# Kernel tuning notes

Hardware: AMD Instinct MI355X
Metric: run time of the kernel (lower is better)

## Reference

```python
import jax, jax.numpy as jnp
import numpy as np

BN_EPS = 1e-5


def spmm(rows, cols, vals, x):
    # Sparse [V,V] @ x for x: [B, V, F]. COO (rows, cols, vals) with E nnz.
    B, V, F = x.shape
    xt = jnp.transpose(x, (1, 0, 2)).reshape(V, B * F)      # [V, B*F]
    msg = xt[cols] * vals[:, None]                           # [E, B*F]
    y = jax.ops.segment_sum(msg, rows, num_segments=V)       # [V, B*F]
    return jnp.transpose(y.reshape(V, B, F), (1, 0, 2))      # [B, V, F]


def cheb_conv(rows, cols, vals, x, W, b):
    # Chebyshev graph conv: out = sum_k T_k(L) x @ W[k] + b ; W: [K, Fin, Fout]
    K = W.shape[0]
    x0 = x
    out = jnp.einsum('bvi,io->bvo', x0, W[0])
    if K > 1:
        x1 = spmm(rows, cols, vals, x0)
        out = out + jnp.einsum('bvi,io->bvo', x1, W[1])
        for k in range(2, K):
            x2 = 2.0 * spmm(rows, cols, vals, x1) - x0
            out = out + jnp.einsum('bvi,io->bvo', x2, W[k])
            x0, x1 = x1, x2
    return out + b


def bn_relu(x, gamma, beta):
    # BatchNorm1d (training stats) over (batch, nodes) per channel, then ReLU.
    m = jnp.mean(x, axis=(0, 1))
    v = jnp.var(x, axis=(0, 1))
    y = (x - m) * jax.lax.rsqrt(v + BN_EPS) * gamma + beta
    return jax.nn.relu(y)


def setup_inputs() -> dict:
    key = jax.random.key(0)
    ks = jax.random.split(key, 8)
    V, DEG, B, CIN, COUT = 49152, 20, 2, 128, 64
    x = jax.random.normal(ks[0], (B, V, CIN), dtype=jnp.float32)
    # HEALPix-like sparse Laplacian: diagonal + 20 random neighbors per node
    self_idx = jnp.arange(V, dtype=jnp.int32)
    nbr = jax.random.randint(ks[1], (V * DEG,), 0, V, dtype=jnp.int32)
    rows = jnp.concatenate([self_idx, jnp.repeat(self_idx, DEG)])
    cols = jnp.concatenate([self_idx, nbr])
    vals = jax.random.normal(ks[2], (V * (DEG + 1),), dtype=jnp.float32) * 0.1
    def w(k, shape):
        fan_in = shape[0] * shape[1]
        return jax.random.normal(k, shape, dtype=jnp.float32) * np.float32(np.sqrt(2.0 / fan_in))
    return {
        'x': x, 'rows': rows, 'cols': cols, 'vals': vals,
        'W1': w(ks[3], (1, CIN, COUT)), 'b1': jnp.zeros((COUT,), jnp.float32),
        'g1': jnp.ones((COUT,), jnp.float32), 'be1': jnp.zeros((COUT,), jnp.float32),
        'W2': w(ks[4], (3, COUT, COUT)), 'b2': jnp.zeros((COUT,), jnp.float32),
        'g2': jnp.ones((COUT,), jnp.float32), 'be2': jnp.zeros((COUT,), jnp.float32),
        'W3': w(ks[5], (1, COUT, CIN)), 'b3': jnp.zeros((CIN,), jnp.float32),
        'g3': jnp.ones((CIN,), jnp.float32), 'be3': jnp.zeros((CIN,), jnp.float32),
    }


def reference(x, rows, cols, vals, W1, b1, g1, be1, W2, b2, g2, be2, W3, b3, g3, be3):
    h = bn_relu(cheb_conv(rows, cols, vals, x, W1, b1), g1, be1)   # [B,V,64]
    h = bn_relu(cheb_conv(rows, cols, vals, h, W2, b2), g2, be2)   # [B,V,64]
    h = bn_relu(cheb_conv(rows, cols, vals, h, W3, b3), g3, be3)   # [B,V,128]
    return h
```

## Files before the change

### kernel.cpp

```cpp
#include <hip/hip_runtime.h>

#define VN 49152
#define DEG 20
#define NB 2
#define MROWS (NB * VN)

static constexpr float BN_EPS = 1e-5f;

typedef short bf16x8 __attribute__((ext_vector_type(8)));
typedef float floatx4 __attribute__((ext_vector_type(4)));

__device__ __forceinline__ unsigned short f2bf(float f) {
  unsigned int u = __builtin_bit_cast(unsigned int, f);
  u += 0x7FFFu + ((u >> 16) & 1u);
  return (unsigned short)(u >> 16);
}
__device__ __forceinline__ float bf2f(unsigned short h) {
  unsigned int u = ((unsigned int)h) << 16;
  return __builtin_bit_cast(float, u);
}
__device__ __forceinline__ float bflo(unsigned int u) {
  return __builtin_bit_cast(float, u << 16);
}
__device__ __forceinline__ float bfhi(unsigned int u) {
  return __builtin_bit_cast(float, u & 0xFFFF0000u);
}
__device__ __forceinline__ unsigned int packbf(float a, float b) {
  return (unsigned int)f2bf(a) | ((unsigned int)f2bf(b) << 16);
}


#define LDA1 136
__global__ __launch_bounds__(256) void gemm1(const float* __restrict__ X,
    const float* __restrict__ W, const float* __restrict__ bias,
    unsigned short* __restrict__ Y, float* __restrict__ part) {
  __shared__ unsigned short As[128 * LDA1];
  __shared__ unsigned short Bs[64 * LDA1];
  __shared__ float sred[128];
  int t = threadIdx.x;
  int row0 = blockIdx.x * 128;
  if (t < 128) sred[t] = 0.f;
  const float* Xt = X + (size_t)row0 * 128;
  #pragma unroll
  for (int c = 0; c < 16; ++c) {
    int f4i = c * 256 + t;
    int row = f4i >> 5, k = (f4i & 31) * 4;
    float4 v = *(const float4*)(Xt + row * 128 + k);
    unsigned int p0 = packbf(v.x, v.y);
    unsigned int p1 = packbf(v.z, v.w);
    *(uint2*)(&As[row * LDA1 + k]) = make_uint2(p0, p1);
  }
  #pragma unroll
  for (int c = 0; c < 32; ++c) {
    int f = c * 256 + t;
    int k = f >> 6, n = f & 63;
    Bs[n * LDA1 + k] = f2bf(W[f]);
  }
  __syncthreads();
  int l = t & 63, wv = t >> 6;
  int lr = l & 15, q = l >> 4;
  int m0 = wv * 32;
  floatx4 acc[2][4];
  #pragma unroll
  for (int mi = 0; mi < 2; ++mi)
    #pragma unroll
    for (int ni = 0; ni < 4; ++ni) acc[mi][ni] = (floatx4)(0.f);
  #pragma unroll
  for (int ks = 0; ks < 128; ks += 32) {
    bf16x8 af[2], bfr[4];
    #pragma unroll
    for (int mi = 0; mi < 2; ++mi)
      af[mi] = *(const bf16x8*)(&As[(m0 + mi * 16 + lr) * LDA1 + ks + q * 8]);
    #pragma unroll
    for (int ni = 0; ni < 4; ++ni)
      bfr[ni] = *(const bf16x8*)(&Bs[(ni * 16 + lr) * LDA1 + ks + q * 8]);
    #pragma unroll
    for (int mi = 0; mi < 2; ++mi)
      #pragma unroll
      for (int ni = 0; ni < 4; ++ni)
        acc[mi][ni] = __builtin_amdgcn_mfma_f32_16x16x32_bf16(af[mi], bfr[ni], acc[mi][ni], 0, 0, 0);
  }
  int b = (row0 >= VN) ? 1 : 0;
  int vbase = row0 - b * VN + m0;
  #pragma unroll
  for (int ni = 0; ni < 4; ++ni) {
    int col = ni * 16 + lr;
    float bv = bias[col];
    size_t sub = (size_t)(b * 2 + (col >> 5)) * VN;
    float s = 0.f, s2 = 0.f;
    #pragma unroll
    for (int mi = 0; mi < 2; ++mi)
      #pragma unroll
      for (int r = 0; r < 4; ++r) {
        float y = acc[mi][ni][r] + bv;
        s += y; s2 += y * y;
        int v = vbase + mi * 16 + q * 4 + r;
        Y[(sub + v) * 32 + (col & 31)] = f2bf(y);
      }
    atomicAdd(&sred[col], s);
    atomicAdd(&sred[64 + col], s2);
  }
  __syncthreads();
  if (t < 128) part[(size_t)blockIdx.x * 128 + t] = sred[t];
}

#define LDA2 72
__global__ __launch_bounds__(256) void gemm2(const unsigned short* __restrict__ X0,
    const unsigned short* __restrict__ X1, const unsigned short* __restrict__ X2,
    const float* __restrict__ W, const float* __restrict__ bias,
    unsigned short* __restrict__ Y, float* __restrict__ part) {
  __shared__ unsigned short As[128 * LDA2];
  __shared__ unsigned short Bs[64 * LDA2];
  __shared__ float sred[128];
  int t = threadIdx.x;
  int row0 = blockIdx.x * 128;
  int b = (row0 >= VN) ? 1 : 0;
  int b2 = b * 2;
  int vb0 = row0 - b * VN;
  if (t < 128) sred[t] = 0.f;
  int l = t & 63, wv = t >> 6;
  int lr = l & 15, q = l >> 4;
  int m0 = wv * 32;
  floatx4 acc[2][4];
  #pragma unroll
  for (int mi = 0; mi < 2; ++mi)
    #pragma unroll
    for (int ni = 0; ni < 4; ++ni) acc[mi][ni] = (floatx4)(0.f);

  for (int term = 0; term < 3; ++term) {
    const unsigned short* Xp = (term == 0) ? X0 : (term == 1) ? X1 : X2;
    const float* Wt = W + term * 64 * 64;
    #pragma unroll
    for (int c8 = 0; c8 < 8; ++c8) {
      int i = c8 * 256 + t;
      int row = i >> 4, k = (i & 15) * 4;
      const unsigned short* src = Xp + ((size_t)(b2 + (k >> 5)) * VN + vb0 + row) * 32 + (k & 31);
      *(uint2*)(&As[row * LDA2 + k]) = *(const uint2*)src;
    }
    #pragma unroll
    for (int c = 0; c < 16; ++c) {
      int f = c * 256 + t;
      int k = f >> 6, n = f & 63;
      Bs[n * LDA2 + k] = f2bf(Wt[f]);
    }
    __syncthreads();
    #pragma unroll
    for (int ks = 0; ks < 64; ks += 32) {
      bf16x8 af[2], bfr[4];
      #pragma unroll
      for (int mi = 0; mi < 2; ++mi)
        af[mi] = *(const bf16x8*)(&As[(m0 + mi * 16 + lr) * LDA2 + ks + q * 8]);
      #pragma unroll
      for (int ni = 0; ni < 4; ++ni)
        bfr[ni] = *(const bf16x8*)(&Bs[(ni * 16 + lr) * LDA2 + ks + q * 8]);
      #pragma unroll
      for (int mi = 0; mi < 2; ++mi)
        #pragma unroll
        for (int ni = 0; ni < 4; ++ni)
          acc[mi][ni] = __builtin_amdgcn_mfma_f32_16x16x32_bf16(af[mi], bfr[ni], acc[mi][ni], 0, 0, 0);
    }
    __syncthreads();
  }
  int vbase = vb0 + m0;
  #pragma unroll
  for (int ni = 0; ni < 4; ++ni) {
    int col = ni * 16 + lr;
    float bv = bias[col];
    size_t sub = (size_t)(b2 + (col >> 5)) * VN;
    float s = 0.f, s2 = 0.f;
    #pragma unroll
    for (int mi = 0; mi < 2; ++mi)
      #pragma unroll
      for (int r = 0; r < 4; ++r) {
        float y = acc[mi][ni][r] + bv;
        s += y; s2 += y * y;
        int v = vbase + mi * 16 + q * 4 + r;
        Y[(sub + v) * 32 + (col & 31)] = f2bf(y);
      }
    atomicAdd(&sred[col], s);
    atomicAdd(&sred[64 + col], s2);
  }
  __syncthreads();
  if (t < 128) part[(size_t)blockIdx.x * 128 + t] = sred[t];
}

__global__ __launch_bounds__(256) void gemm3(const unsigned short* __restrict__ X,
    const float* __restrict__ W, const float* __restrict__ bias,
    const float* __restrict__ scsh, unsigned short* __restrict__ Y,
    float* __restrict__ part) {
  __shared__ unsigned short As[128 * LDA2];
  __shared__ unsigned short Bs[64 * LDA2];
  __shared__ float sred[128];
  int t = threadIdx.x;
  int row0 = blockIdx.x * 128;
  int n0 = blockIdx.y * 64;
  int b = (row0 >= VN) ? 1 : 0;
  int b2 = b * 2;
  int vb0 = row0 - b * VN;
  if (t < 128) sred[t] = 0.f;
  #pragma unroll
  for (int c8 = 0; c8 < 8; ++c8) {
    int i = c8 * 256 + t;
    int row = i >> 4, k = (i & 15) * 4;
    const unsigned short* src = X + ((size_t)(b2 + (k >> 5)) * VN + vb0 + row) * 32 + (k & 31);
    uint2 rawv = *(const uint2*)src;
    float y0 = fmaf(bflo(rawv.x), scsh[k + 0], scsh[64 + k + 0]);
    float y1 = fmaf(bfhi(rawv.x), scsh[k + 1], scsh[64 + k + 1]);
    float y2 = fmaf(bflo(rawv.y), scsh[k + 2], scsh[64 + k + 2]);
    float y3 = fmaf(bfhi(rawv.y), scsh[k + 3], scsh[64 + k + 3]);
    y0 = y0 > 0.f ? y0 : 0.f; y1 = y1 > 0.f ? y1 : 0.f;
    y2 = y2 > 0.f ? y2 : 0.f; y3 = y3 > 0.f ? y3 : 0.f;
    *(uint2*)(&As[row * LDA2 + k]) = make_uint2(packbf(y0, y1), packbf(y2, y3));
  }
  #pragma unroll
  for (int c = 0; c < 16; ++c) {
    int f = c * 256 + t;
    int k = f >> 6, n = f & 63;
    Bs[n * LDA2 + k] = f2bf(W[k * 128 + n0 + n]);
  }
  __syncthreads();
  int l = t & 63, wv = t >> 6;
  int lr = l & 15, q = l >> 4;
  int m0 = wv * 32;
  floatx4 acc[2][4];
  #pragma unroll
  for (int mi = 0; mi < 2; ++mi)
    #pragma unroll
    for (int ni = 0; ni < 4; ++ni) acc[mi][ni] = (floatx4)(0.f);
  #pragma unroll
  for (int ks = 0; ks < 64; ks += 32) {
    bf16x8 af[2], bfr[4];
    #pragma unroll
    for (int mi = 0; mi < 2; ++mi)
      af[mi] = *(const bf16x8*)(&As[(m0 + mi * 16 + lr) * LDA2 + ks + q * 8]);
    #pragma unroll
    for (int ni = 0; ni < 4; ++ni)
      bfr[ni] = *(const bf16x8*)(&Bs[(ni * 16 + lr) * LDA2 + ks + q * 8]);
    #pragma unroll
    for (int mi = 0; mi < 2; ++mi)
      #pragma unroll
      for (int ni = 0; ni < 4; ++ni)
        acc[mi][ni] = __builtin_amdgcn_mfma_f32_16x16x32_bf16(af[mi], bfr[ni], acc[mi][ni], 0, 0, 0);
  }
  #pragma unroll
  for (int ni = 0; ni < 4; ++ni) {
    int lc = ni * 16 + lr;
    int col = n0 + lc;
    float bv = bias[col];
    float s = 0.f, s2 = 0.f;
    #pragma unroll
    for (int mi = 0; mi < 2; ++mi)
      #pragma unroll
      for (int r = 0; r < 4; ++r) {
        float y = acc[mi][ni][r] + bv;
        s += y; s2 += y * y;
        int row = row0 + m0 + mi * 16 + q * 4 + r;
        Y[(size_t)row * 128 + col] = f2bf(y);
      }
    atomicAdd(&sred[lc], s);
    atomicAdd(&sred[64 + lc], s2);
  }
  __syncthreads();
  if (t < 128)
    part[((size_t)blockIdx.y * 768 + blockIdx.x) * 128 + t] = sred[t];
}

__global__ __launch_bounds__(128) void reduce_scsh64(const float* __restrict__ part,
    const float* __restrict__ gamma, const float* __restrict__ beta,
    float* __restrict__ scsh) {
  int t = threadIdx.x;
  const float* p = part + t;
  float a0 = 0.f, a1 = 0.f, a2 = 0.f, a3 = 0.f;
  for (int b = 0; b < 768; b += 4) {
    a0 += p[(size_t)(b + 0) * 128]; a1 += p[(size_t)(b + 1) * 128];
    a2 += p[(size_t)(b + 2) * 128]; a3 += p[(size_t)(b + 3) * 128];
  }
  __shared__ float sm[128];
  sm[t] = (a0 + a1) + (a2 + a3);
  __syncthreads();
  if (t < 64) {
    float mean = sm[t] * (1.f / MROWS);
    float var = sm[64 + t] * (1.f / MROWS) - mean * mean;
    float sc = gamma[t] * rsqrtf(var + BN_EPS);
    scsh[t] = sc;
    scsh[64 + t] = beta[t] - mean * sc;
  }
}

__global__ __launch_bounds__(256) void reduce_scsh128(const float* __restrict__ part,
    const float* __restrict__ gamma, const float* __restrict__ beta,
    float* __restrict__ scsh) {
  int t = threadIdx.x;
  int col = t & 127, s = t >> 7;
  int gy = col >> 6, lc = col & 63;
  const float* p = part + (size_t)gy * 768 * 128 + s * 64 + lc;
  float a0 = 0.f, a1 = 0.f, a2 = 0.f, a3 = 0.f;
  for (int gx = 0; gx < 768; gx += 4) {
    a0 += p[(size_t)(gx + 0) * 128]; a1 += p[(size_t)(gx + 1) * 128];
    a2 += p[(size_t)(gx + 2) * 128]; a3 += p[(size_t)(gx + 3) * 128];
  }
  __shared__ float sm[256];
  sm[s * 128 + col] = (a0 + a1) + (a2 + a3);
  __syncthreads();
  if (t < 128) {
    float mean = sm[t] * (1.f / MROWS);
    float var = sm[128 + t] * (1.f / MROWS) - mean * mean;
    float sc = gamma[t] * rsqrtf(var + BN_EPS);
    scsh[t] = sc;
    scsh[128 + t] = beta[t] - mean * sc;
  }
}

__global__ __launch_bounds__(256) void bn_h1(const unsigned short* __restrict__ T1,
    const float* __restrict__ scsh, unsigned short* __restrict__ H1) {
  int g = blockIdx.x;
  int combo = (g & 7) >> 1;
  int rg = ((g >> 3) << 1) | (g & 1);
  int t = threadIdx.x;
  int wv = t >> 6, lane = t & 63;
  int v = rg * 64 + wv * 16 + (lane >> 2);
  int ch0 = (lane & 3) * 8;
  int cb = (combo & 1) * 32 + ch0;
  size_t off = (size_t)combo * VN * 32 + (size_t)v * 32 + ch0;
  uint4 d = *(const uint4*)(T1 + off);
  float y[8];
  y[0] = fmaf(bflo(d.x), scsh[cb + 0], scsh[64 + cb + 0]);
  y[1] = fmaf(bfhi(d.x), scsh[cb + 1], scsh[64 + cb + 1]);
  y[2] = fmaf(bflo(d.y), scsh[cb + 2], scsh[64 + cb + 2]);
  y[3] = fmaf(bfhi(d.y), scsh[cb + 3], scsh[64 + cb + 3]);
  y[4] = fmaf(bflo(d.z), scsh[cb + 4], scsh[64 + cb + 4]);
  y[5] = fmaf(bfhi(d.z), scsh[cb + 5], scsh[64 + cb + 5]);
  y[6] = fmaf(bflo(d.w), scsh[cb + 6], scsh[64 + cb + 6]);
  y[7] = fmaf(bfhi(d.w), scsh[cb + 7], scsh[64 + cb + 7]);
  #pragma unroll
  for (int j = 0; j < 8; ++j) y[j] = y[j] > 0.f ? y[j] : 0.f;
  uint4 o;
  o.x = packbf(y[0], y[1]); o.y = packbf(y[2], y[3]);
  o.z = packbf(y[4], y[5]); o.w = packbf(y[6], y[7]);
  *(uint4*)(H1 + off) = o;
}

__global__ __launch_bounds__(256) void spmm1(const unsigned short* __restrict__ H1,
    const int* __restrict__ cols, const float* __restrict__ vals,
    unsigned short* __restrict__ X1out) {
  int g = blockIdx.x;
  int combo = (g & 7) >> 1;
  int rg = ((g >> 3) << 1) | (g & 1);
  int t = threadIdx.x;
  int wv = t >> 6, lane = t & 63;
  int v = rg * 64 + wv * 16 + (lane >> 2);
  int ch0 = (lane & 3) * 8;
  const unsigned short* __restrict__ plane = H1 + (size_t)combo * VN * 32;
  float a[8];
  {
    float w0 = vals[v];
    uint4 d = *(const uint4*)(plane + (size_t)v * 32 + ch0);
    a[0] = w0 * bflo(d.x); a[1] = w0 * bfhi(d.x);
    a[2] = w0 * bflo(d.y); a[3] = w0 * bfhi(d.y);
    a[4] = w0 * bflo(d.z); a[5] = w0 * bfhi(d.z);
    a[6] = w0 * bflo(d.w); a[7] = w0 * bfhi(d.w);
  }
  const int*   __restrict__ cp = cols + VN + v * DEG;
  const float* __restrict__ vp = vals + VN + v * DEG;
  #pragma unroll
  for (int j = 0; j < DEG; ++j) {
    int cj = cp[j];
    float wj = vp[j];
    uint4 d = *(const uint4*)(plane + (size_t)cj * 32 + ch0);
    a[0] = fmaf(bflo(d.x), wj, a[0]); a[1] = fmaf(bfhi(d.x), wj, a[1]);
    a[2] = fmaf(bflo(d.y), wj, a[2]); a[3] = fmaf(bfhi(d.y), wj, a[3]);
    a[4] = fmaf(bflo(d.z), wj, a[4]); a[5] = fmaf(bfhi(d.z), wj, a[5]);
    a[6] = fmaf(bflo(d.w), wj, a[6]); a[7] = fmaf(bfhi(d.w), wj, a[7]);
  }
  uint4 o;
  o.x = packbf(a[0], a[1]); o.y = packbf(a[2], a[3]);
  o.z = packbf(a[4], a[5]); o.w = packbf(a[6], a[7]);
  *(uint4*)(X1out + (size_t)combo * VN * 32 + (size_t)v * 32 + ch0) = o;
}

__global__ __launch_bounds__(256) void spmm2(const unsigned short* __restrict__ X1,
    const unsigned short* __restrict__ H1, const int* __restrict__ cols,
    const float* __restrict__ vals, unsigned short* __restrict__ X2out) {
  int g = blockIdx.x;
  int combo = (g & 7) >> 1;
  int rg = ((g >> 3) << 1) | (g & 1);
  int t = threadIdx.x;
  int wv = t >> 6, lane = t & 63;
  int v = rg * 64 + wv * 16 + (lane >> 2);
  int ch0 = (lane & 3) * 8;
  const size_t pbase = (size_t)combo * VN * 32;
  const size_t myoff = pbase + (size_t)v * 32 + ch0;
  const unsigned short* __restrict__ plane = X1 + pbase;
  float a[8];
  {
    float w0 = vals[v];
    uint4 d = *(const uint4*)(X1 + myoff);
    a[0] = w0 * bflo(d.x); a[1] = w0 * bfhi(d.x);
    a[2] = w0 * bflo(d.y); a[3] = w0 * bfhi(d.y);
    a[4] = w0 * bflo(d.z); a[5] = w0 * bfhi(d.z);
    a[6] = w0 * bflo(d.w); a[7] = w0 * bfhi(d.w);
  }
  const int*   __restrict__ cp = cols + VN + v * DEG;
  const float* __restrict__ vp = vals + VN + v * DEG;
  #pragma unroll
  for (int j = 0; j < DEG; ++j) {
    int cj = cp[j];
    float wj = vp[j];
    uint4 d = *(const uint4*)(plane + (size_t)cj * 32 + ch0);
    a[0] = fmaf(bflo(d.x), wj, a[0]); a[1] = fmaf(bfhi(d.x), wj, a[1]);
    a[2] = fmaf(bflo(d.y), wj, a[2]); a[3] = fmaf(bfhi(d.y), wj, a[3]);
    a[4] = fmaf(bflo(d.z), wj, a[4]); a[5] = fmaf(bfhi(d.z), wj, a[5]);
    a[6] = fmaf(bflo(d.w), wj, a[6]); a[7] = fmaf(bfhi(d.w), wj, a[7]);
  }
  uint4 h = *(const uint4*)(H1 + myoff);
  float hh[8] = {bflo(h.x), bfhi(h.x), bflo(h.y), bfhi(h.y),
                 bflo(h.z), bfhi(h.z), bflo(h.w), bfhi(h.w)};
  uint4 o;
  o.x = packbf(2.f * a[0] - hh[0], 2.f * a[1] - hh[1]);
  o.y = packbf(2.f * a[2] - hh[2], 2.f * a[3] - hh[3]);
  o.z = packbf(2.f * a[4] - hh[4], 2.f * a[5] - hh[5]);
  o.w = packbf(2.f * a[6] - hh[6], 2.f * a[7] - hh[7]);
  *(uint4*)(X2out + myoff) = o;
}

__global__ __launch_bounds__(256) void bn_apply_final(const unsigned short* __restrict__ T,
    float* __restrict__ Y, const float* __restrict__ scsh) {
  size_t i4 = ((size_t)blockIdx.x * 256 + threadIdx.x) * 4;
  int c0 = (int)(i4 & 127);
  ushort4 tv = *(const ushort4*)(T + i4);
  unsigned short sv[4] = {tv.x, tv.y, tv.z, tv.w};
  float ov[4];
  #pragma unroll
  for (int j = 0; j < 4; ++j) {
    int c = c0 + j;
    float y = fmaf(bf2f(sv[j]), scsh[c], scsh[128 + c]);
    ov[j] = y > 0.f ? y : 0.f;
  }
  *(float4*)(Y + i4) = make_float4(ov[0], ov[1], ov[2], ov[3]);
}

extern "C" void kernel_launch(void* const* d_in, const int* in_sizes, int n_in,
                              void* d_out, int out_size, void* d_ws, size_t ws_size,
                              hipStream_t stream) {
  const float* x    = (const float*)d_in[0];
  const int*   cols = (const int*)  d_in[2];
  const float* vals = (const float*)d_in[3];
  const float* W1   = (const float*)d_in[4];
  const float* b1   = (const float*)d_in[5];
  const float* g1   = (const float*)d_in[6];
  const float* be1  = (const float*)d_in[7];
  const float* W2   = (const float*)d_in[8];
  const float* b2   = (const float*)d_in[9];
  const float* g2   = (const float*)d_in[10];
  const float* be2  = (const float*)d_in[11];
  const float* W3   = (const float*)d_in[12];
  const float* b3   = (const float*)d_in[13];
  const float* g3   = (const float*)d_in[14];
  const float* be3  = (const float*)d_in[15];
  float* out = (float*)d_out;

  const size_t PL = (size_t)MROWS * 64;
  unsigned short* P0 = (unsigned short*)d_ws;
  unsigned short* PH = P0 + PL;
  unsigned short* P1 = PH + PL;
  unsigned short* P2 = P1 + PL;
  float* part  = (float*)(P2 + 2 * PL);
  float* scsh1 = part + 1536 * 128;
  float* scsh2 = scsh1 + 128;
  float* scsh3 = scsh2 + 128;

  dim3 blk(256);
  int rowb = MROWS / 128;
  int spmm_blocks = 3072;
  int ap128_blocks = (int)(PL * 2 / 4 / 256);

  gemm1<<<rowb, blk, 0, stream>>>(x, W1, b1, P0, part);
  reduce_scsh64<<<1, 128, 0, stream>>>(part, g1, be1, scsh1);
  bn_h1<<<spmm_blocks, blk, 0, stream>>>(P0, scsh1, PH);

  spmm1<<<spmm_blocks, blk, 0, stream>>>(PH, cols, vals, P1);
  spmm2<<<spmm_blocks, blk, 0, stream>>>(P1, PH, cols, vals, P2);
  gemm2<<<rowb, blk, 0, stream>>>(PH, P1, P2, W2, b2, P0, part);
  reduce_scsh64<<<1, 128, 0, stream>>>(part, g2, be2, scsh2);

  dim3 g3grid(rowb, 2);
  gemm3<<<g3grid, blk, 0, stream>>>(P0, W3, b3, scsh2, P2, part);
  reduce_scsh128<<<1, 256, 0, stream>>>(part, g3, be3, scsh3);
  bn_apply_final<<<ap128_blocks, blk, 0, stream>>>(P2, out, scsh3);
}
```

Measured before the change: 285.8 us.

## Fuse BN statistics and BN-ReLU application into the GEMM and SpMM kernels

Each GEMM now reduces its BN statistics with global atomics, and the last block to finish computes scale and shift. This removes the separate reduce kernels and the per-block partials buffer. The standalone bn_h1 pass is dropped: spmm1, spmm2 and gemm2 apply BN+ReLU on the fly to the raw GEMM1 output, so the normalized buffer is never written or read again. gemm3 now computes all 128 output columns per block instead of splitting them over two grid columns, which avoids loading the A tile twice. In exchange, spmm1 redoes the BN+ReLU arithmetic on every gathered neighbor. Float atomics make the summation order nondeterministic, and gemm2 writes its output in place over one of its own inputs.

```diff
diff --git a/kernel.cpp b/kernel.cpp
--- a/kernel.cpp
+++ b/kernel.cpp
@@ -33,10 +33,13 @@
 #define LDA1 136
 __global__ __launch_bounds__(256) void gemm1(const float* __restrict__ X,
     const float* __restrict__ W, const float* __restrict__ bias,
-    unsigned short* __restrict__ Y, float* __restrict__ part) {
+    const float* __restrict__ gamma, const float* __restrict__ beta,
+    unsigned short* __restrict__ Y, float* __restrict__ gsum,
+    int* __restrict__ counter, float* __restrict__ scshOut) {
   __shared__ unsigned short As[128 * LDA1];
   __shared__ unsigned short Bs[64 * LDA1];
   __shared__ float sred[128];
+  __shared__ int amLast;
   int t = threadIdx.x;
   int row0 = blockIdx.x * 128;
   if (t < 128) sred[t] = 0.f;
@@ -101,218 +104,27 @@
     atomicAdd(&sred[64 + col], s2);
   }
   __syncthreads();
-  if (t < 128) part[(size_t)blockIdx.x * 128 + t] = sred[t];
-}
-
-#define LDA2 72
-__global__ __launch_bounds__(256) void gemm2(const unsigned short* __restrict__ X0,
-    const unsigned short* __restrict__ X1, const unsigned short* __restrict__ X2,
-    const float* __restrict__ W, const float* __restrict__ bias,
-    unsigned short* __restrict__ Y, float* __restrict__ part) {
-  __shared__ unsigned short As[128 * LDA2];
-  __shared__ unsigned short Bs[64 * LDA2];
-  __shared__ float sred[128];
-  int t = threadIdx.x;
-  int row0 = blockIdx.x * 128;
-  int b = (row0 >= VN) ? 1 : 0;
-  int b2 = b * 2;
-  int vb0 = row0 - b * VN;
-  if (t < 128) sred[t] = 0.f;
-  int l = t & 63, wv = t >> 6;
-  int lr = l & 15, q = l >> 4;
-  int m0 = wv * 32;
-  floatx4 acc[2][4];
-  #pragma unroll
-  for (int mi = 0; mi < 2; ++mi)
-    #pragma unroll
-    for (int ni = 0; ni < 4; ++ni) acc[mi][ni] = (floatx4)(0.f);
-
-  for (int term = 0; term < 3; ++term) {
-    const unsigned short* Xp = (term == 0) ? X0 : (term == 1) ? X1 : X2;
-    const float* Wt = W + term * 64 * 64;
-    #pragma unroll
-    for (int c8 = 0; c8 < 8; ++c8) {
-      int i = c8 * 256 + t;
-      int row = i >> 4, k = (i & 15) * 4;
-      const unsigned short* src = Xp + ((size_t)(b2 + (k >> 5)) * VN + vb0 + row) * 32 + (k & 31);
-      *(uint2*)(&As[row * LDA2 + k]) = *(const uint2*)src;
-    }
-    #pragma unroll
-    for (int c = 0; c < 16; ++c) {
-      int f = c * 256 + t;
-      int k = f >> 6, n = f & 63;
-      Bs[n * LDA2 + k] = f2bf(Wt[f]);
-    }
-    __syncthreads();
-    #pragma unroll
-    for (int ks = 0; ks < 64; ks += 32) {
-      bf16x8 af[2], bfr[4];
-      #pragma unroll
-      for (int mi = 0; mi < 2; ++mi)
-        af[mi] = *(const bf16x8*)(&As[(m0 + mi * 16 + lr) * LDA2 + ks + q * 8]);
-      #pragma unroll
-      for (int ni = 0; ni < 4; ++ni)
-        bfr[ni] = *(const bf16x8*)(&Bs[(ni * 16 + lr) * LDA2 + ks + q * 8]);
-      #pragma unroll
-      for (int mi = 0; mi < 2; ++mi)
-        #pragma unroll
-        for (int ni = 0; ni < 4; ++ni)
-          acc[mi][ni] = __builtin_amdgcn_mfma_f32_16x16x32_bf16(af[mi], bfr[ni], acc[mi][ni], 0, 0, 0);
-    }
-    __syncthreads();
-  }
-  int vbase = vb0 + m0;
-  #pragma unroll
-  for (int ni = 0; ni < 4; ++ni) {
-    int col = ni * 16 + lr;
-    float bv = bias[col];
-    size_t sub = (size_t)(b2 + (col >> 5)) * VN;
-    float s = 0.f, s2 = 0.f;
-    #pragma unroll
-    for (int mi = 0; mi < 2; ++mi)
-      #pragma unroll
-      for (int r = 0; r < 4; ++r) {
-        float y = acc[mi][ni][r] + bv;
-        s += y; s2 += y * y;
-        int v = vbase + mi * 16 + q * 4 + r;
-        Y[(sub + v) * 32 + (col & 31)] = f2bf(y);
-      }
-    atomicAdd(&sred[col], s);
-    atomicAdd(&sred[64 + col], s2);
-  }
-  __syncthreads();
-  if (t < 128) part[(size_t)blockIdx.x * 128 + t] = sred[t];
-}
-
-__global__ __launch_bounds__(256) void gemm3(const unsigned short* __restrict__ X,
-    const float* __restrict__ W, const float* __restrict__ bias,
-    const float* __restrict__ scsh, unsigned short* __restrict__ Y,
-    float* __restrict__ part) {
-  __shared__ unsigned short As[128 * LDA2];
-  __shared__ unsigned short Bs[64 * LDA2];
-  __shared__ float sred[128];
-  int t = threadIdx.x;
-  int row0 = blockIdx.x * 128;
-  int n0 = blockIdx.y * 64;
-  int b = (row0 >= VN) ? 1 : 0;
-  int b2 = b * 2;
-  int vb0 = row0 - b * VN;
-  if (t < 128) sred[t] = 0.f;
-  #pragma unroll
-  for (int c8 = 0; c8 < 8; ++c8) {
-    int i = c8 * 256 + t;
-    int row = i >> 4, k = (i & 15) * 4;
-    const unsigned short* src = X + ((size_t)(b2 + (k >> 5)) * VN + vb0 + row) * 32 + (k & 31);
-    uint2 rawv = *(const uint2*)src;
-    float y0 = fmaf(bflo(rawv.x), scsh[k + 0], scsh[64 + k + 0]);
-    float y1 = fmaf(bfhi(rawv.x), scsh[k + 1], scsh[64 + k + 1]);
-    float y2 = fmaf(bflo(rawv.y), scsh[k + 2], scsh[64 + k + 2]);
-    float y3 = fmaf(bfhi(rawv.y), scsh[k + 3], scsh[64 + k + 3]);
-    y0 = y0 > 0.f ? y0 : 0.f; y1 = y1 > 0.f ? y1 : 0.f;
-    y2 = y2 > 0.f ? y2 : 0.f; y3 = y3 > 0.f ? y3 : 0.f;
-    *(uint2*)(&As[row * LDA2 + k]) = make_uint2(packbf(y0, y1), packbf(y2, y3));
-  }
-  #pragma unroll
-  for (int c = 0; c < 16; ++c) {
-    int f = c * 256 + t;
-    int k = f >> 6, n = f & 63;
-    Bs[n * LDA2 + k] = f2bf(W[k * 128 + n0 + n]);
-  }
-  __syncthreads();
-  int l = t & 63, wv = t >> 6;
-  int lr = l & 15, q = l >> 4;
-  int m0 = wv * 32;
-  floatx4 acc[2][4];
-  #pragma unroll
-  for (int mi = 0; mi < 2; ++mi)
-    #pragma unroll
-    for (int ni = 0; ni < 4; ++ni) acc[mi][ni] = (floatx4)(0.f);
-  #pragma unroll
-  for (int ks = 0; ks < 64; ks += 32) {
-    bf16x8 af[2], bfr[4];
-    #pragma unroll
-    for (int mi = 0; mi < 2; ++mi)
-      af[mi] = *(const bf16x8*)(&As[(m0 + mi * 16 + lr) * LDA2 + ks + q * 8]);
-    #pragma unroll
-    for (int ni = 0; ni < 4; ++ni)
-      bfr[ni] = *(const bf16x8*)(&Bs[(ni * 16 + lr) * LDA2 + ks + q * 8]);
-    #pragma unroll
-    for (int mi = 0; mi < 2; ++mi)
-      #pragma unroll
-      for (int ni = 0; ni < 4; ++ni)
-        acc[mi][ni] = __builtin_amdgcn_mfma_f32_16x16x32_bf16(af[mi], bfr[ni], acc[mi][ni], 0, 0, 0);
-  }
-  #pragma unroll
-  for (int ni = 0; ni < 4; ++ni) {
-    int lc = ni * 16 + lr;
-    int col = n0 + lc;
-    float bv = bias[col];
-    float s = 0.f, s2 = 0.f;
-    #pragma unroll
-    for (int mi = 0; mi < 2; ++mi)
-      #pragma unroll
-      for (int r = 0; r < 4; ++r) {
-        float y = acc[mi][ni][r] + bv;
-        s += y; s2 += y * y;
-        int row = row0 + m0 + mi * 16 + q * 4 + r;
-        Y[(size_t)row * 128 + col] = f2bf(y);
-      }
-    atomicAdd(&sred[lc], s);
-    atomicAdd(&sred[64 + lc], s2);
-  }
-  __syncthreads();
-  if (t < 128)
-    part[((size_t)blockIdx.y * 768 + blockIdx.x) * 128 + t] = sred[t];
-}
-
-__global__ __launch_bounds__(128) void reduce_scsh64(const float* __restrict__ part,
-    const float* __restrict__ gamma, const float* __restrict__ beta,
-    float* __restrict__ scsh) {
-  int t = threadIdx.x;
-  const float* p = part + t;
-  float a0 = 0.f, a1 = 0.f, a2 = 0.f, a3 = 0.f;
-  for (int b = 0; b < 768; b += 4) {
-    a0 += p[(size_t)(b + 0) * 128]; a1 += p[(size_t)(b + 1) * 128];
-    a2 += p[(size_t)(b + 2) * 128]; a3 += p[(size_t)(b + 3) * 128];
-  }
-  __shared__ float sm[128];
-  sm[t] = (a0 + a1) + (a2 + a3);
-  __syncthreads();
-  if (t < 64) {
-    float mean = sm[t] * (1.f / MROWS);
-    float var = sm[64 + t] * (1.f / MROWS) - mean * mean;
+  if (t < 128) atomicAdd(&gsum[t], sred[t]);
+  __syncthreads();
+  if (t == 0) {
+    __threadfence();
+    amLast = (atomicAdd(counter, 1) == (int)gridDim.x - 1) ? 1 : 0;
+  }
+  __syncthreads();
+  if (amLast && t < 64) {
+    float s  = atomicAdd(&gsum[t], 0.f);
+    float s2 = atomicAdd(&gsum[64 + t], 0.f);
+    float mean = s * (1.f / MROWS);
+    float var  = s2 * (1.f / MROWS) - mean * mean;
     float sc = gamma[t] * rsqrtf(var + BN_EPS);
-    scsh[t] = sc;
-    scsh[64 + t] = beta[t] - mean * sc;
-  }
-}
-
-__global__ __launch_bounds__(256) void reduce_scsh128(const float* __restrict__ part,
-    const float* __restrict__ gamma, const float* __restrict__ beta,
-    float* __restrict__ scsh) {
-  int t = threadIdx.x;
-  int col = t & 127, s = t >> 7;
-  int gy = col >> 6, lc = col & 63;
-  const float* p = part + (size_t)gy * 768 * 128 + s * 64 + lc;
-  float a0 = 0.f, a1 = 0.f, a2 = 0.f, a3 = 0.f;
-  for (int gx = 0; gx < 768; gx += 4) {
-    a0 += p[(size_t)(gx + 0) * 128]; a1 += p[(size_t)(gx + 1) * 128];
-    a2 += p[(size_t)(gx + 2) * 128]; a3 += p[(size_t)(gx + 3) * 128];
-  }
-  __shared__ float sm[256];
-  sm[s * 128 + col] = (a0 + a1) + (a2 + a3);
-  __syncthreads();
-  if (t < 128) {
-    float mean = sm[t] * (1.f / MROWS);
-    float var = sm[128 + t] * (1.f / MROWS) - mean * mean;
-    float sc = gamma[t] * rsqrtf(var + BN_EPS);
-    scsh[t] = sc;
-    scsh[128 + t] = beta[t] - mean * sc;
-  }
-}
-
-__global__ __launch_bounds__(256) void bn_h1(const unsigned short* __restrict__ T1,
-    const float* __restrict__ scsh, unsigned short* __restrict__ H1) {
+    scshOut[t] = sc;
+    scshOut[64 + t] = beta[t] - mean * sc;
+  }
+}
+
+__global__ __launch_bounds__(256) void spmm1(const unsigned short* __restrict__ T1,
+    const int* __restrict__ cols, const float* __restrict__ vals,
+    const float* __restrict__ scsh, unsigned short* __restrict__ X1out) {
   int g = blockIdx.x;
   int combo = (g & 7) >> 1;
   int rg = ((g >> 3) << 1) | (g & 1);
@@ -321,44 +133,22 @@
   int v = rg * 64 + wv * 16 + (lane >> 2);
   int ch0 = (lane & 3) * 8;
   int cb = (combo & 1) * 32 + ch0;
-  size_t off = (size_t)combo * VN * 32 + (size_t)v * 32 + ch0;
-  uint4 d = *(const uint4*)(T1 + off);
-  float y[8];
-  y[0] = fmaf(bflo(d.x), scsh[cb + 0], scsh[64 + cb + 0]);
-  y[1] = fmaf(bfhi(d.x), scsh[cb + 1], scsh[64 + cb + 1]);
-  y[2] = fmaf(bflo(d.y), scsh[cb + 2], scsh[64 + cb + 2]);
-  y[3] = fmaf(bfhi(d.y), scsh[cb + 3], scsh[64 + cb + 3]);
-  y[4] = fmaf(bflo(d.z), scsh[cb + 4], scsh[64 + cb + 4]);
-  y[5] = fmaf(bfhi(d.z), scsh[cb + 5], scsh[64 + cb + 5]);
-  y[6] = fmaf(bflo(d.w), scsh[cb + 6], scsh[64 + cb + 6]);
-  y[7] = fmaf(bfhi(d.w), scsh[cb + 7], scsh[64 + cb + 7]);
-  #pragma unroll
-  for (int j = 0; j < 8; ++j) y[j] = y[j] > 0.f ? y[j] : 0.f;
-  uint4 o;
-  o.x = packbf(y[0], y[1]); o.y = packbf(y[2], y[3]);
-  o.z = packbf(y[4], y[5]); o.w = packbf(y[6], y[7]);
-  *(uint4*)(H1 + off) = o;
-}
-
-__global__ __launch_bounds__(256) void spmm1(const unsigned short* __restrict__ H1,
-    const int* __restrict__ cols, const float* __restrict__ vals,
-    unsigned short* __restrict__ X1out) {
-  int g = blockIdx.x;
-  int combo = (g & 7) >> 1;
-  int rg = ((g >> 3) << 1) | (g & 1);
-  int t = threadIdx.x;
-  int wv = t >> 6, lane = t & 63;
-  int v = rg * 64 + wv * 16 + (lane >> 2);
-  int ch0 = (lane & 3) * 8;
-  const unsigned short* __restrict__ plane = H1 + (size_t)combo * VN * 32;
+  float sc[8], sh[8];
+  #pragma unroll
+  for (int j = 0; j < 8; ++j) { sc[j] = scsh[cb + j]; sh[j] = scsh[64 + cb + j]; }
+  const unsigned short* __restrict__ plane = T1 + (size_t)combo * VN * 32;
   float a[8];
   {
     float w0 = vals[v];
     uint4 d = *(const uint4*)(plane + (size_t)v * 32 + ch0);
-    a[0] = w0 * bflo(d.x); a[1] = w0 * bfhi(d.x);
-    a[2] = w0 * bflo(d.y); a[3] = w0 * bfhi(d.y);
-    a[4] = w0 * bflo(d.z); a[5] = w0 * bfhi(d.z);
-    a[6] = w0 * bflo(d.w); a[7] = w0 * bfhi(d.w);
+    float e[8] = {bflo(d.x), bfhi(d.x), bflo(d.y), bfhi(d.y),
+                  bflo(d.z), bfhi(d.z), bflo(d.w), bfhi(d.w)};
+    #pragma unroll
+    for (int j = 0; j < 8; ++j) {
+      float h = fmaf(e[j], sc[j], sh[j]);
+      h = h > 0.f ? h : 0.f;
+      a[j] = w0 * h;
+    }
   }
   const int*   __restrict__ cp = cols + VN + v * DEG;
   const float* __restrict__ vp = vals + VN + v * DEG;
@@ -367,10 +157,14 @@
     int cj = cp[j];
     float wj = vp[j];
     uint4 d = *(const uint4*)(plane + (size_t)cj * 32 + ch0);
-    a[0] = fmaf(bflo(d.x), wj, a[0]); a[1] = fmaf(bfhi(d.x), wj, a[1]);
-    a[2] = fmaf(bflo(d.y), wj, a[2]); a[3] = fmaf(bfhi(d.y), wj, a[3]);
-    a[4] = fmaf(bflo(d.z), wj, a[4]); a[5] = fmaf(bfhi(d.z), wj, a[5]);
-    a[6] = fmaf(bflo(d.w), wj, a[6]); a[7] = fmaf(bfhi(d.w), wj, a[7]);
+    float e[8] = {bflo(d.x), bfhi(d.x), bflo(d.y), bfhi(d.y),
+                  bflo(d.z), bfhi(d.z), bflo(d.w), bfhi(d.w)};
+    #pragma unroll
+    for (int i = 0; i < 8; ++i) {
+      float h = fmaf(e[i], sc[i], sh[i]);
+      h = h > 0.f ? h : 0.f;
+      a[i] = fmaf(h, wj, a[i]);
+    }
   }
   uint4 o;
   o.x = packbf(a[0], a[1]); o.y = packbf(a[2], a[3]);
@@ -379,8 +173,9 @@
 }
 
 __global__ __launch_bounds__(256) void spmm2(const unsigned short* __restrict__ X1,
-    const unsigned short* __restrict__ H1, const int* __restrict__ cols,
-    const float* __restrict__ vals, unsigned short* __restrict__ X2out) {
+    const unsigned short* __restrict__ T1, const int* __restrict__ cols,
+    const float* __restrict__ vals, const float* __restrict__ scsh,
+    unsigned short* __restrict__ X2out) {
   int g = blockIdx.x;
   int combo = (g & 7) >> 1;
   int rg = ((g >> 3) << 1) | (g & 1);
@@ -412,15 +207,241 @@
     a[4] = fmaf(bflo(d.z), wj, a[4]); a[5] = fmaf(bfhi(d.z), wj, a[5]);
     a[6] = fmaf(bflo(d.w), wj, a[6]); a[7] = fmaf(bfhi(d.w), wj, a[7]);
   }
-  uint4 h = *(const uint4*)(H1 + myoff);
-  float hh[8] = {bflo(h.x), bfhi(h.x), bflo(h.y), bfhi(h.y),
-                 bflo(h.z), bfhi(h.z), bflo(h.w), bfhi(h.w)};
+  int cb = (combo & 1) * 32 + ch0;
+  float sc[8], sh[8];
+  #pragma unroll
+  for (int j = 0; j < 8; ++j) { sc[j] = scsh[cb + j]; sh[j] = scsh[64 + cb + j]; }
+  uint4 hr = *(const uint4*)(T1 + myoff);
+  float e[8] = {bflo(hr.x), bfhi(hr.x), bflo(hr.y), bfhi(hr.y),
+                bflo(hr.z), bfhi(hr.z), bflo(hr.w), bfhi(hr.w)};
+  float oo[8];
+  #pragma unroll
+  for (int j = 0; j < 8; ++j) {
+    float h = fmaf(e[j], sc[j], sh[j]);
+    h = h > 0.f ? h : 0.f;
+    oo[j] = 2.f * a[j] - h;
+  }
   uint4 o;
-  o.x = packbf(2.f * a[0] - hh[0], 2.f * a[1] - hh[1]);
-  o.y = packbf(2.f * a[2] - hh[2], 2.f * a[3] - hh[3]);
-  o.z = packbf(2.f * a[4] - hh[4], 2.f * a[5] - hh[5]);
-  o.w = packbf(2.f * a[6] - hh[6], 2.f * a[7] - hh[7]);
+  o.x = packbf(oo[0], oo[1]); o.y = packbf(oo[2], oo[3]);
+  o.z = packbf(oo[4], oo[5]); o.w = packbf(oo[6], oo[7]);
   *(uint4*)(X2out + myoff) = o;
+}
+
+#define LDA2 72
+__global__ __launch_bounds__(256) void gemm2(const unsigned short* X0,
+    const unsigned short* __restrict__ X1, const unsigned short* __restrict__ X2,
+    const float* __restrict__ W, const float* __restrict__ bias,
+    const float* __restrict__ scsh, const float* __restrict__ gamma,
+    const float* __restrict__ beta, unsigned short* Y,
+    float* __restrict__ gsum, int* __restrict__ counter,
+    float* __restrict__ scshOut) {
+  __shared__ unsigned short As[128 * LDA2];
+  __shared__ unsigned short Bs[64 * LDA2];
+  __shared__ float sred[128];
+  __shared__ int amLast;
+  int t = threadIdx.x;
+  int row0 = blockIdx.x * 128;
+  int b = (row0 >= VN) ? 1 : 0;
+  int b2 = b * 2;
+  int vb0 = row0 - b * VN;
+  if (t < 128) sred[t] = 0.f;
+  int kk = (t & 15) * 4;
+  int r0 = t >> 4;
+  float tsc[4], tsh[4];
+  #pragma unroll
+  for (int j = 0; j < 4; ++j) { tsc[j] = scsh[kk + j]; tsh[j] = scsh[64 + kk + j]; }
+  int l = t & 63, wv = t >> 6;
+  int lr = l & 15, q = l >> 4;
+  int m0 = wv * 32;
+  floatx4 acc[2][4];
+  #pragma unroll
+  for (int mi = 0; mi < 2; ++mi)
+    #pragma unroll
+    for (int ni = 0; ni < 4; ++ni) acc[mi][ni] = (floatx4)(0.f);
+
+  #pragma unroll
+  for (int term = 0; term < 3; ++term) {
+    const unsigned short* Xp = (term == 0) ? X0 : (term == 1) ? X1 : X2;
+    const float* Wt = W + term * 64 * 64;
+    const unsigned short* srcBase =
+        Xp + ((size_t)(b2 + (kk >> 5)) * VN + vb0) * 32 + (kk & 31);
+    #pragma unroll
+    for (int c8 = 0; c8 < 8; ++c8) {
+      int row = c8 * 16 + r0;
+      uint2 rawv = *(const uint2*)(srcBase + (size_t)row * 32);
+      if (term == 0) {
+        float y0 = fmaf(bflo(rawv.x), tsc[0], tsh[0]);
+        float y1 = fmaf(bfhi(rawv.x), tsc[1], tsh[1]);
+        float y2 = fmaf(bflo(rawv.y), tsc[2], tsh[2]);
+        float y3 = fmaf(bfhi(rawv.y), tsc[3], tsh[3]);
+        y0 = y0 > 0.f ? y0 : 0.f; y1 = y1 > 0.f ? y1 : 0.f;
+        y2 = y2 > 0.f ? y2 : 0.f; y3 = y3 > 0.f ? y3 : 0.f;
+        *(uint2*)(&As[row * LDA2 + kk]) = make_uint2(packbf(y0, y1), packbf(y2, y3));
+      } else {
+        *(uint2*)(&As[row * LDA2 + kk]) = rawv;
+      }
+    }
+    #pragma unroll
+    for (int c = 0; c < 16; ++c) {
+      int f = c * 256 + t;
+      int k = f >> 6, n = f & 63;
+      Bs[n * LDA2 + k] = f2bf(Wt[f]);
+    }
+    __syncthreads();
+    #pragma unroll
+    for (int ks = 0; ks < 64; ks += 32) {
+      bf16x8 af[2], bfr[4];
+      #pragma unroll
+      for (int mi = 0; mi < 2; ++mi)
+        af[mi] = *(const bf16x8*)(&As[(m0 + mi * 16 + lr) * LDA2 + ks + q * 8]);
+      #pragma unroll
+      for (int ni = 0; ni < 4; ++ni)
+        bfr[ni] = *(const bf16x8*)(&Bs[(ni * 16 + lr) * LDA2 + ks + q * 8]);
+      #pragma unroll
+      for (int mi = 0; mi < 2; ++mi)
+        #pragma unroll
+        for (int ni = 0; ni < 4; ++ni)
+          acc[mi][ni] = __builtin_amdgcn_mfma_f32_16x16x32_bf16(af[mi], bfr[ni], acc[mi][ni], 0, 0, 0);
+    }
+    __syncthreads();
+  }
+  int vbase = vb0 + m0;
+  #pragma unroll
+  for (int ni = 0; ni < 4; ++ni) {
+    int col = ni * 16 + lr;
+    float bv = bias[col];
+    size_t sub = (size_t)(b2 + (col >> 5)) * VN;
+    float s = 0.f, s2 = 0.f;
+    #pragma unroll
+    for (int mi = 0; mi < 2; ++mi)
+      #pragma unroll
+      for (int r = 0; r < 4; ++r) {
+        float y = acc[mi][ni][r] + bv;
+        s += y; s2 += y * y;
+        int v = vbase + mi * 16 + q * 4 + r;
+        Y[(sub + v) * 32 + (col & 31)] = f2bf(y);
+      }
+    atomicAdd(&sred[col], s);
+    atomicAdd(&sred[64 + col], s2);
+  }
+  __syncthreads();
+  if (t < 128) atomicAdd(&gsum[t], sred[t]);
+  __syncthreads();
+  if (t == 0) {
+    __threadfence();
+    amLast = (atomicAdd(counter, 1) == (int)gridDim.x - 1) ? 1 : 0;
+  }
+  __syncthreads();
+  if (amLast && t < 64) {
+    float s  = atomicAdd(&gsum[t], 0.f);
+    float s2 = atomicAdd(&gsum[64 + t], 0.f);
+    float mean = s * (1.f / MROWS);
+    float var  = s2 * (1.f / MROWS) - mean * mean;
+    float sc = gamma[t] * rsqrtf(var + BN_EPS);
+    scshOut[t] = sc;
+    scshOut[64 + t] = beta[t] - mean * sc;
+  }
+}
+
+__global__ __launch_bounds__(256) void gemm3(const unsigned short* __restrict__ X,
+    const float* __restrict__ W, const float* __restrict__ bias,
+    const float* __restrict__ scsh, const float* __restrict__ gamma,
+    const float* __restrict__ beta, unsigned short* __restrict__ Y,
+    float* __restrict__ gsum, int* __restrict__ counter,
+    float* __restrict__ scshOut) {
+  __shared__ unsigned short As[128 * LDA2];
+  __shared__ unsigned short Bs[128 * LDA2];
+  __shared__ float sred[256];
+  __shared__ int amLast;
+  int t = threadIdx.x;
+  int row0 = blockIdx.x * 128;
+  int b = (row0 >= VN) ? 1 : 0;
+  int b2 = b * 2;
+  int vb0 = row0 - b * VN;
+  sred[t] = 0.f;
+  int kk = (t & 15) * 4;
+  int r0 = t >> 4;
+  float tsc[4], tsh[4];
+  #pragma unroll
+  for (int j = 0; j < 4; ++j) { tsc[j] = scsh[kk + j]; tsh[j] = scsh[64 + kk + j]; }
+  const unsigned short* srcBase =
+      X + ((size_t)(b2 + (kk >> 5)) * VN + vb0) * 32 + (kk & 31);
+  #pragma unroll
+  for (int c8 = 0; c8 < 8; ++c8) {
+    int row = c8 * 16 + r0;
+    uint2 rawv = *(const uint2*)(srcBase + (size_t)row * 32);
+    float y0 = fmaf(bflo(rawv.x), tsc[0], tsh[0]);
+    float y1 = fmaf(bfhi(rawv.x), tsc[1], tsh[1]);
+    float y2 = fmaf(bflo(rawv.y), tsc[2], tsh[2]);
+    float y3 = fmaf(bfhi(rawv.y), tsc[3], tsh[3]);
+    y0 = y0 > 0.f ? y0 : 0.f; y1 = y1 > 0.f ? y1 : 0.f;
+    y2 = y2 > 0.f ? y2 : 0.f; y3 = y3 > 0.f ? y3 : 0.f;
+    *(uint2*)(&As[row * LDA2 + kk]) = make_uint2(packbf(y0, y1), packbf(y2, y3));
+  }
+  #pragma unroll
+  for (int c = 0; c < 32; ++c) {
+    int f = c * 256 + t;
+    int k = f >> 7, n = f & 127;
+    Bs[n * LDA2 + k] = f2bf(W[k * 128 + n]);
+  }
+  __syncthreads();
+  int l = t & 63, wv = t >> 6;
+  int lr = l & 15, q = l >> 4;
+  int m0 = wv * 32;
+  floatx4 acc[2][8];
+  #pragma unroll
+  for (int mi = 0; mi < 2; ++mi)
+    #pragma unroll
+    for (int ni = 0; ni < 8; ++ni) acc[mi][ni] = (floatx4)(0.f);
+  #pragma unroll
+  for (int ks = 0; ks < 64; ks += 32) {
+    bf16x8 af[2], bfr[8];
+    #pragma unroll
+    for (int mi = 0; mi < 2; ++mi)
+      af[mi] = *(const bf16x8*)(&As[(m0 + mi * 16 + lr) * LDA2 + ks + q * 8]);
+    #pragma unroll
+    for (int ni = 0; ni < 8; ++ni)
+      bfr[ni] = *(const bf16x8*)(&Bs[(ni * 16 + lr) * LDA2 + ks + q * 8]);
+    #pragma unroll
+    for (int mi = 0; mi < 2; ++mi)
+      #pragma unroll
+      for (int ni = 0; ni < 8; ++ni)
+        acc[mi][ni] = __builtin_amdgcn_mfma_f32_16x16x32_bf16(af[mi], bfr[ni], acc[mi][ni], 0, 0, 0);
+  }
+  #pragma unroll
+  for (int ni = 0; ni < 8; ++ni) {
+    int col = ni * 16 + lr;
+    float bv = bias[col];
+    float s = 0.f, s2 = 0.f;
+    #pragma unroll
+    for (int mi = 0; mi < 2; ++mi)
+      #pragma unroll
+      for (int r = 0; r < 4; ++r) {
+        float y = acc[mi][ni][r] + bv;
+        s += y; s2 += y * y;
+        int row = row0 + m0 + mi * 16 + q * 4 + r;
+        Y[(size_t)row * 128 + col] = f2bf(y);
+      }
+    atomicAdd(&sred[col], s);
+    atomicAdd(&sred[128 + col], s2);
+  }
+  __syncthreads();
+  atomicAdd(&gsum[t], sred[t]);
+  __syncthreads();
+  if (t == 0) {
+    __threadfence();
+    amLast = (atomicAdd(counter, 1) == (int)gridDim.x - 1) ? 1 : 0;
+  }
+  __syncthreads();
+  if (amLast && t < 128) {
+    float s  = atomicAdd(&gsum[t], 0.f);
+    float s2 = atomicAdd(&gsum[128 + t], 0.f);
+    float mean = s * (1.f / MROWS);
+    float var  = s2 * (1.f / MROWS) - mean * mean;
+    float sc = gamma[t] * rsqrtf(var + BN_EPS);
+    scshOut[t] = sc;
+    scshOut[128 + t] = beta[t] - mean * sc;
+  }
 }
 
 __global__ __launch_bounds__(256) void bn_apply_final(const unsigned short* __restrict__ T,
@@ -461,30 +482,30 @@
 
   const size_t PL = (size_t)MROWS * 64;
   unsigned short* P0 = (unsigned short*)d_ws;
-  unsigned short* PH = P0 + PL;
-  unsigned short* P1 = PH + PL;
+  unsigned short* P1 = P0 + PL;
   unsigned short* P2 = P1 + PL;
-  float* part  = (float*)(P2 + 2 * PL);
-  float* scsh1 = part + 1536 * 128;
+  float* ctrl  = (float*)(P2 + 2 * PL);
+  float* gsum1 = ctrl;
+  float* gsum2 = ctrl + 128;
+  float* gsum3 = ctrl + 256;
+  int*   cnts  = (int*)(ctrl + 512);
+  float* scsh1 = ctrl + 516;
   float* scsh2 = scsh1 + 128;
   float* scsh3 = scsh2 + 128;
+
+  hipMemsetAsync(ctrl, 0, 516 * sizeof(float), stream);
 
   dim3 blk(256);
   int rowb = MROWS / 128;
   int spmm_blocks = 3072;
   int ap128_blocks = (int)(PL * 2 / 4 / 256);
 
-  gemm1<<<rowb, blk, 0, stream>>>(x, W1, b1, P0, part);
-  reduce_scsh64<<<1, 128, 0, stream>>>(part, g1, be1, scsh1);
-  bn_h1<<<spmm_blocks, blk, 0, stream>>>(P0, scsh1, PH);
-
-  spmm1<<<spmm_blocks, blk, 0, stream>>>(PH, cols, vals, P1);
-  spmm2<<<spmm_blocks, blk, 0, stream>>>(P1, PH, cols, vals, P2);
-  gemm2<<<rowb, blk, 0, stream>>>(PH, P1, P2, W2, b2, P0, part);
-  reduce_scsh64<<<1, 128, 0, stream>>>(part, g2, be2, scsh2);
-
-  dim3 g3grid(rowb, 2);
-  gemm3<<<g3grid, blk, 0, stream>>>(P0, W3, b3, scsh2, P2, part);
-  reduce_scsh128<<<1, 256, 0, stream>>>(part, g3, be3, scsh3);
+  gemm1<<<rowb, blk, 0, stream>>>(x, W1, b1, g1, be1, P0, gsum1, cnts + 0, scsh1);
+
+  spmm1<<<spmm_blocks, blk, 0, stream>>>(P0, cols, vals, scsh1, P1);
+  spmm2<<<spmm_blocks, blk, 0, stream>>>(P1, P0, cols, vals, scsh1, P2);
+  gemm2<<<rowb, blk, 0, stream>>>(P0, P1, P2, W2, b2, scsh1, g2, be2, P0, gsum2, cnts + 1, scsh2);
+
+  gemm3<<<rowb, blk, 0, stream>>>(P0, W3, b3, scsh2, g3, be3, P2, gsum3, cnts + 2, scsh3);
   bn_apply_final<<<ap128_blocks, blk, 0, stream>>>(P2, out, scsh3);
 }
```

New measurement: 337.3 us. 18.0% more time.
